# Kernel optimization log

Measured on AMD Instinct MI355X. Metric: run time of the kernel, lower is better.

The kernel has to match this reference:

```python
import jax, jax.numpy as jnp
import numpy as np

FACTOR = 1  # init factor -> top_k = int(factor * log(L))


def setup_inputs() -> dict:
    key = jax.random.key(0)
    kq, kk, kv = jax.random.split(key, 3)
    B, L, H, E = 16, 2048, 8, 64
    shape = (B, L, H, E)
    return {
        "queries": jax.random.normal(kq, shape, dtype=jnp.float32),
        "keys": jax.random.normal(kk, shape, dtype=jnp.float32),
        "values": jax.random.normal(kv, shape, dtype=jnp.float32),
    }


def reference(queries, keys, values):
    B, L, H, E = queries.shape
    # seq lens equal -> torch's pad/truncate branch is a no-op slice
    q = jnp.transpose(queries, (0, 2, 3, 1))  # [B,H,E,L]
    k = jnp.transpose(keys, (0, 2, 3, 1))
    v = jnp.transpose(values, (0, 2, 3, 1))

    # FFT-based circular cross-correlation along time
    qf = jnp.fft.rfft(q, axis=-1)
    kf = jnp.fft.rfft(k, axis=-1)
    corr = jnp.fft.irfft(qf * jnp.conj(kf), n=L, axis=-1)  # [B,H,E,L]

    top_k = int(FACTOR * np.log(L))  # static: 7 for L=2048
    mean_value = corr.mean(axis=(1, 2))  # mean over head then variates -> [B,L]
    # global (batch-averaged) top-k delays, shared across batch (training path)
    _, topk_index = jax.lax.top_k(mean_value.mean(axis=0), top_k)  # [k]
    # per-batch weights at those delays, softmax over k
    w = jax.nn.softmax(mean_value[:, topk_index], axis=-1)  # [B,k]

    # torch.roll(v, -d, -1)[..., t] == v[..., (t + d) % L]
    idx = (jnp.arange(L)[None, :] + topk_index[:, None]) % L  # [k,L]
    gathered = v[..., idx]  # [B,H,E,k,L]
    agg = jnp.einsum('bhekl,bk->bhel', gathered, w)  # weighted delay aggregation

    return jnp.transpose(agg, (0, 3, 1, 2))  # back to [B,L,H,E]
```

## Files before the change

kernel.cpp:

```cpp
#include <hip/hip_runtime.h>
#include <hip/hip_bf16.h>
#include <hip/hip_fp16.h>
#include <math.h>


#define B_ 16
#define L_ 2048
#define H_ 8
#define E_ 64
#define K_ 7
#define RS_ 2178

#define Z_OFF    0ull
#define PART_OFF 67108864ull
#define S_OFF    (PART_OFF + 33554432ull)
#define MV_OFF   (S_OFF + 262144ull)
#define TK_OFF   (MV_OFF + 131072ull)
#define W_OFF    (TK_OFF + 64ull)

__device__ __forceinline__ float2 cadd(float2 a, float2 b) { return make_float2(a.x + b.x, a.y + b.y); }
__device__ __forceinline__ float2 csub(float2 a, float2 b) { return make_float2(a.x - b.x, a.y - b.y); }
__device__ __forceinline__ float2 cmul(float2 a, float2 b) {
  return make_float2(fmaf(a.x, b.x, -a.y * b.y), fmaf(a.x, b.y, a.y * b.x));
}
__device__ __forceinline__ float2 cis(float ang) { float s, c; sincosf(ang, &s, &c); return make_float2(c, s); }

template<int S> __device__ __forceinline__ float2 rot90(float2 z) {
  return (S < 0) ? make_float2(z.y, -z.x) : make_float2(-z.y, z.x);
}
template<int S> __device__ __forceinline__ void dft4(float2& a, float2& b, float2& c, float2& d) {
  float2 t0 = cadd(a, c), t1 = csub(a, c), t2 = cadd(b, d), t3 = rot90<S>(csub(b, d));
  a = cadd(t0, t2); c = csub(t0, t2); b = cadd(t1, t3); d = csub(t1, t3);
}
template<int S> __device__ __forceinline__ void dft8(float2 v[8]) {
  const float RT = 0.70710678118654752f;
  const float SR = (S < 0) ? -RT : RT;
  float2 a0 = cadd(v[0], v[4]), a1 = cadd(v[1], v[5]), a2 = cadd(v[2], v[6]), a3 = cadd(v[3], v[7]);
  float2 b0 = csub(v[0], v[4]), b1 = csub(v[1], v[5]), b2 = csub(v[2], v[6]), b3 = csub(v[3], v[7]);
  b1 = cmul(b1, make_float2(RT, SR));
  b2 = rot90<S>(b2);
  b3 = cmul(b3, make_float2(-RT, SR));
  dft4<S>(a0, a1, a2, a3);
  dft4<S>(b0, b1, b2, b3);
  v[0] = a0; v[2] = a1; v[4] = a2; v[6] = a3;
  v[1] = b0; v[3] = b1; v[5] = b2; v[7] = b3;
}
__device__ __forceinline__ int sg(int e) { return e + (e >> 4); }

struct hc { __half2 re, im; };
__device__ __forceinline__ hc hcadd(hc a, hc b) { return { __hadd2(a.re, b.re), __hadd2(a.im, b.im) }; }
__device__ __forceinline__ hc hcsub(hc a, hc b) { return { __hsub2(a.re, b.re), __hsub2(a.im, b.im) }; }
template<int S> __device__ __forceinline__ hc hrot90(hc z) {
  hc r; if (S < 0) { r.re = z.im; r.im = __hneg2(z.re); } else { r.re = __hneg2(z.im); r.im = z.re; }
  return r;
}
__device__ __forceinline__ hc hcmul(hc v, __half2 wre, __half2 wim) {
  hc r;
  r.re = __hsub2(__hmul2(v.re, wre), __hmul2(v.im, wim));
  r.im = __hfma2(v.re, wim, __hmul2(v.im, wre));
  return r;
}
template<int S> __device__ __forceinline__ void hdft4(hc& a, hc& b, hc& c, hc& d) {
  hc t0 = hcadd(a, c), t1 = hcsub(a, c), t2 = hcadd(b, d), t3 = hrot90<S>(hcsub(b, d));
  a = hcadd(t0, t2); c = hcsub(t0, t2); b = hcadd(t1, t3); d = hcsub(t1, t3);
}
template<int S> __device__ __forceinline__ void hdft8(hc v[8]) {
  const float RT = 0.70710678118654752f;
  __half2 rt  = __float2half2_rn(RT);
  __half2 sr  = __float2half2_rn((S < 0) ? -RT : RT);
  __half2 nrt = __float2half2_rn(-RT);
  hc a0 = hcadd(v[0], v[4]), a1 = hcadd(v[1], v[5]), a2 = hcadd(v[2], v[6]), a3 = hcadd(v[3], v[7]);
  hc b0 = hcsub(v[0], v[4]), b1 = hcsub(v[1], v[5]), b2 = hcsub(v[2], v[6]), b3 = hcsub(v[3], v[7]);
  b1 = hcmul(b1, rt, sr);
  b2 = hrot90<S>(b2);
  b3 = hcmul(b3, nrt, sr);
  hdft4<S>(a0, a1, a2, a3);
  hdft4<S>(b0, b1, b2, b3);
  v[0] = a0; v[2] = a1; v[4] = a2; v[6] = a3;
  v[1] = b0; v[3] = b1; v[5] = b2; v[7] = b3;
}
__device__ __forceinline__ __half2 u2h(unsigned u) { return __builtin_bit_cast(__half2, u); }
__device__ __forceinline__ unsigned h2u(__half2 h) { return __builtin_bit_cast(unsigned, h); }

__global__ __launch_bounds__(512) void pack_kernel(
    const float* __restrict__ q, const float* __restrict__ k,
    float4* __restrict__ z) {
  int tid = threadIdx.x;
  int l = blockIdx.x;
  int tl = l & 63, b = l >> 6;
  size_t rowbase = ((size_t)b * L_ + tl * 32) * 512;
  const float4* q4 = (const float4*)(q + rowbase);
  const float4* k4 = (const float4*)(k + rowbase);
  float4* slab = z + (size_t)l * 4096;
  int w = tid >> 6;
  int lane = tid & 63;
  int r = lane >> 3, c = lane & 7;
  int srcLane = ((lane & 7) << 3) | (lane >> 3);
#pragma unroll
  for (int i = 0; i < 8; ++i) {
    int s = w * 8 + i;
    int tr = s & 3, cc = s >> 2;
    int ridx = (tr * 8 + r) * 128 + cc * 8 + c;
    float4 qv = q4[ridx];
    float4 kv = k4[ridx];
    float4 pk;
    ((__half2*)&pk)[0] = __float22half2_rn(make_float2(qv.x, qv.y));
    ((__half2*)&pk)[1] = __float22half2_rn(make_float2(kv.x, kv.y));
    ((__half2*)&pk)[2] = __float22half2_rn(make_float2(qv.z, qv.w));
    ((__half2*)&pk)[3] = __float22half2_rn(make_float2(kv.z, kv.w));
    float4 tp;
    tp.x = __shfl(pk.x, srcLane, 64);
    tp.y = __shfl(pk.y, srcLane, 64);
    tp.z = __shfl(pk.z, srcLane, 64);
    tp.w = __shfl(pk.w, srcLane, 64);
    slab[(cc * 8 + (lane >> 3)) * 32 + tr * 8 + (lane & 7)] = tp;
  }
}

__global__ __launch_bounds__(256, 4) void fft_corr_kernel(
    const float4* __restrict__ z, float2* __restrict__ part) {
  extern __shared__ uint2 dbuf[];
  int t = threadIdx.x;
  int j2 = t & 31, j3 = t & 3;
  int l = blockIdx.x;
  int cg = l & 127, b = l >> 7;
  const float4* zb = z + (size_t)b * 64 * 4096;

#pragma unroll
  for (int it = 0; it < 8; ++it) {
    int m = it * 256 + t;
    int tl = m >> 5, j = m & 31;
    float4 pk = zb[(size_t)tl * 4096 + cg * 32 + j];
    int sp = sg(tl * 32 + j);
    dbuf[sp]       = make_uint2(__float_as_uint(pk.x), __float_as_uint(pk.y));
    dbuf[RS_ + sp] = make_uint2(__float_as_uint(pk.z), __float_as_uint(pk.w));
  }

  __half2 t1re[7], t1im[7], t2re[7], t2im[7], t3re[7], t3im[7];
  {
    float2 w1 = cis(-6.283185307179586f * (float)t  / 2048.0f);
    float2 w2 = cis(-6.283185307179586f * (float)j2 / 256.0f);
    float2 w3 = cis(-6.283185307179586f * (float)j3 / 32.0f);
    float2 a1 = w1, a2 = w2, a3 = w3;
#pragma unroll
    for (int kk = 0; kk < 7; ++kk) {
      t1re[kk] = __float2half2_rn(a1.x); t1im[kk] = __float2half2_rn(a1.y);
      t2re[kk] = __float2half2_rn(a2.x); t2im[kk] = __float2half2_rn(a2.y);
      t3re[kk] = __float2half2_rn(a3.x); t3im[kk] = __float2half2_rn(a3.y);
      a1 = cmul(a1, w1); a2 = cmul(a2, w2); a3 = cmul(a3, w3);
    }
  }
  int base2 = (t >> 5) * 256 + j2;
  int base3 = (t >> 2) * 32 + j3;
  uint2* R0 = dbuf;
  uint2* R1 = dbuf + RS_;
  hc v0[8], v1[8];
  __syncthreads();

#pragma unroll
  for (int m = 0; m < 8; ++m) {
    uint2 u = R0[sg(t + 256 * m)]; v0[m].re = u2h(u.x); v0[m].im = u2h(u.y);
    u = R1[sg(t + 256 * m)];       v1[m].re = u2h(u.x); v1[m].im = u2h(u.y);
  }
  hdft8<-1>(v0); hdft8<-1>(v1);
#pragma unroll
  for (int kk = 1; kk < 8; ++kk) {
    v0[kk] = hcmul(v0[kk], t1re[kk - 1], t1im[kk - 1]);
    v1[kk] = hcmul(v1[kk], t1re[kk - 1], t1im[kk - 1]);
  }
#pragma unroll
  for (int kk = 0; kk < 8; ++kk) {
    R0[sg(t + 256 * kk)] = make_uint2(h2u(v0[kk].re), h2u(v0[kk].im));
    R1[sg(t + 256 * kk)] = make_uint2(h2u(v1[kk].re), h2u(v1[kk].im));
  }
  __syncthreads();
#pragma unroll
  for (int m = 0; m < 8; ++m) {
    uint2 u = R0[sg(base2 + 32 * m)]; v0[m].re = u2h(u.x); v0[m].im = u2h(u.y);
    u = R1[sg(base2 + 32 * m)];       v1[m].re = u2h(u.x); v1[m].im = u2h(u.y);
  }
  hdft8<-1>(v0); hdft8<-1>(v1);
#pragma unroll
  for (int kk = 1; kk < 8; ++kk) {
    v0[kk] = hcmul(v0[kk], t2re[kk - 1], t2im[kk - 1]);
    v1[kk] = hcmul(v1[kk], t2re[kk - 1], t2im[kk - 1]);
  }
#pragma unroll
  for (int kk = 0; kk < 8; ++kk) {
    R0[sg(base2 + 32 * kk)] = make_uint2(h2u(v0[kk].re), h2u(v0[kk].im));
    R1[sg(base2 + 32 * kk)] = make_uint2(h2u(v1[kk].re), h2u(v1[kk].im));
  }
  __syncthreads();
#pragma unroll
  for (int m = 0; m < 8; ++m) {
    uint2 u = R0[sg(base3 + 4 * m)]; v0[m].re = u2h(u.x); v0[m].im = u2h(u.y);
    u = R1[sg(base3 + 4 * m)];       v1[m].re = u2h(u.x); v1[m].im = u2h(u.y);
  }
  hdft8<-1>(v0); hdft8<-1>(v1);
#pragma unroll
  for (int kk = 1; kk < 8; ++kk) {
    v0[kk] = hcmul(v0[kk], t3re[kk - 1], t3im[kk - 1]);
    v1[kk] = hcmul(v1[kk], t3re[kk - 1], t3im[kk - 1]);
  }
#pragma unroll
  for (int kk = 0; kk < 8; ++kk) {
    R0[sg(base3 + 4 * kk)] = make_uint2(h2u(v0[kk].re), h2u(v0[kk].im));
    R1[sg(base3 + 4 * kk)] = make_uint2(h2u(v1[kk].re), h2u(v1[kk].im));
  }
  __syncthreads();
#pragma unroll
  for (int kk = 0; kk < 8; ++kk) {
    uint2 u = R0[sg(8 * t + kk)]; v0[kk].re = u2h(u.x); v0[kk].im = u2h(u.y);
    u = R1[sg(8 * t + kk)];       v1[kk].re = u2h(u.x); v1[kk].im = u2h(u.y);
  }
  hdft4<-1>(v0[0], v0[1], v0[2], v0[3]); hdft4<-1>(v0[4], v0[5], v0[6], v0[7]);
  hdft4<-1>(v1[0], v1[1], v1[2], v1[3]); hdft4<-1>(v1[4], v1[5], v1[6], v1[7]);
#pragma unroll
  for (int kk = 0; kk < 8; ++kk) {
    R0[sg(8 * t + kk)] = make_uint2(h2u(v0[kk].re), h2u(v0[kk].im));
    R1[sg(8 * t + kk)] = make_uint2(h2u(v1[kk].re), h2u(v1[kk].im));
  }
  __syncthreads();
  float2 acc[8];
#pragma unroll
  for (int kk = 0; kk < 8; ++kk) {
    int pos = 8 * t + kk;
    int f  = ((pos >> 8) & 7) | (((pos >> 5) & 7) << 3) | (((pos >> 2) & 7) << 6) | ((pos & 3) << 9);
    int fp = (2048 - f) & 2047;
    int pp = ((fp & 7) << 8) | (((fp >> 3) & 7) << 5) | (((fp >> 6) & 7) << 2) | ((fp >> 9) & 3);
    float sx = 0.f, sy = 0.f;
    {
      uint2 ub = R0[sg(pp)];
      __half2 bre = u2h(ub.x), bim = u2h(ub.y);
      float ar0 = __low2float(v0[kk].re),  ar1 = __high2float(v0[kk].re);
      float ai0 = __low2float(v0[kk].im),  ai1 = __high2float(v0[kk].im);
      float br0 = __low2float(bre),        br1 = __high2float(bre);
      float bi0 = __low2float(bim),        bi1 = __high2float(bim);
      sx += (br0 * ai0 + bi0 * ar0) + (br1 * ai1 + bi1 * ar1);
      sy += (ar0 * ar0 + ai0 * ai0 - br0 * br0 - bi0 * bi0)
          + (ar1 * ar1 + ai1 * ai1 - br1 * br1 - bi1 * bi1);
    }
    {
      uint2 ub = R1[sg(pp)];
      __half2 bre = u2h(ub.x), bim = u2h(ub.y);
      float ar0 = __low2float(v1[kk].re),  ar1 = __high2float(v1[kk].re);
      float ai0 = __low2float(v1[kk].im),  ai1 = __high2float(v1[kk].im);
      float br0 = __low2float(bre),        br1 = __high2float(bre);
      float bi0 = __low2float(bim),        bi1 = __high2float(bim);
      sx += (br0 * ai0 + bi0 * ar0) + (br1 * ai1 + bi1 * ar1);
      sy += (ar0 * ar0 + ai0 * ai0 - br0 * br0 - bi0 * bi0)
          + (ar1 * ar1 + ai1 * ai1 - br1 * br1 - bi1 * bi1);
    }
    acc[kk] = make_float2(0.5f * sx, 0.25f * sy);
  }
  __syncthreads();
  {
    float2* pk0 = (float2*)dbuf;
#pragma unroll
    for (int kk = 0; kk < 8; ++kk) pk0[sg(8 * t + kk)] = acc[kk];
  }
  __syncthreads();
  {
    const float2* pk0 = (const float2*)dbuf;
    float2* prow = part + (size_t)l * L_;
#pragma unroll
    for (int m = 0; m < 8; ++m) {
      int p = t + 256 * m;
      prow[p] = pk0[sg(p)];
    }
  }
}

__global__ __launch_bounds__(256) void reduce_S_kernel(
    const float2* __restrict__ part, float2* __restrict__ S) {
  int idx = blockIdx.x * 256 + threadIdx.x;
  int p = idx & 2047;
  int b = idx >> 11;
  float2 s = make_float2(0.f, 0.f);
#pragma unroll 4
  for (int i = 0; i < 128; ++i) {
    float2 vv = part[(size_t)(b * 128 + i) * L_ + p];
    s.x += vv.x; s.y += vv.y;
  }
  S[idx] = s;
}

__global__ __launch_bounds__(256) void ifft_kernel(
    const float2* __restrict__ S, float* __restrict__ mv) {
  __shared__ float2 buf[2176];
  int t = threadIdx.x, b = blockIdx.x;
  int j2 = t & 31, j3 = t & 3;
  float2 tw1[7], tw2[7], tw3[7];
  {
    float2 w1 = cis(6.283185307179586f * (float)t  / 2048.0f);
    float2 w2 = cis(6.283185307179586f * (float)j2 / 256.0f);
    float2 w3 = cis(6.283185307179586f * (float)j3 / 32.0f);
    tw1[0] = w1; tw2[0] = w2; tw3[0] = w3;
#pragma unroll
    for (int kk = 1; kk < 7; ++kk) {
      tw1[kk] = cmul(tw1[kk - 1], w1);
      tw2[kk] = cmul(tw2[kk - 1], w2);
      tw3[kk] = cmul(tw3[kk - 1], w3);
    }
  }
  int base2 = (t >> 5) * 256 + j2;
  int base3 = (t >> 2) * 32 + j3;
  float2 u[8];
  {
    const float4* rp = (const float4*)(S + (size_t)b * L_);
#pragma unroll
    for (int m = 0; m < 4; ++m) {
      float4 f = rp[4 * t + m];
      u[2 * m]     = make_float2(f.x, f.y);
      u[2 * m + 1] = make_float2(f.z, f.w);
    }
  }
  dft4<1>(u[0], u[1], u[2], u[3]);
  dft4<1>(u[4], u[5], u[6], u[7]);
#pragma unroll
  for (int kk = 0; kk < 8; ++kk) buf[sg(8 * t + kk)] = u[kk];
  __syncthreads();
  float2 v[8];
#pragma unroll
  for (int kk = 0; kk < 8; ++kk) v[kk] = buf[sg(base3 + 4 * kk)];
#pragma unroll
  for (int kk = 1; kk < 8; ++kk) v[kk] = cmul(v[kk], tw3[kk - 1]);
  dft8<1>(v);
  __syncthreads();
#pragma unroll
  for (int m = 0; m < 8; ++m) buf[sg(base3 + 4 * m)] = v[m];
  __syncthreads();
#pragma unroll
  for (int kk = 0; kk < 8; ++kk) v[kk] = buf[sg(base2 + 32 * kk)];
#pragma unroll
  for (int kk = 1; kk < 8; ++kk) v[kk] = cmul(v[kk], tw2[kk - 1]);
  dft8<1>(v);
  __syncthreads();
#pragma unroll
  for (int m = 0; m < 8; ++m) buf[sg(base2 + 32 * m)] = v[m];
  __syncthreads();
#pragma unroll
  for (int kk = 0; kk < 8; ++kk) v[kk] = buf[sg(t + 256 * kk)];
#pragma unroll
  for (int kk = 1; kk < 8; ++kk) v[kk] = cmul(v[kk], tw1[kk - 1]);
  dft8<1>(v);
  const float scale = 1.0f / (2048.0f * 512.0f);
#pragma unroll
  for (int m = 0; m < 8; ++m) mv[b * L_ + t + 256 * m] = v[m].x * scale;
}

__global__ __launch_bounds__(256) void topk_kernel(
    const float* __restrict__ mv, int* __restrict__ topk, float* __restrict__ wts) {
  __shared__ float av[2048];
  __shared__ float rv[256];
  __shared__ int   ri[256];
  __shared__ int   sidx[K_];
  int tid = threadIdx.x;
  for (int d = tid; d < 2048; d += 256) {
    float s = 0.f;
#pragma unroll
    for (int b = 0; b < B_; ++b) s += mv[b * L_ + d];
    av[d] = s;
  }
  __syncthreads();
  for (int kk = 0; kk < K_; ++kk) {
    float bv = -INFINITY; int bi = 0;
    for (int d = tid; d < 2048; d += 256) {
      float vv = av[d];
      if (vv > bv) { bv = vv; bi = d; }
    }
    rv[tid] = bv; ri[tid] = bi;
    __syncthreads();
    for (int off = 128; off > 0; off >>= 1) {
      if (tid < off) {
        float v2 = rv[tid + off]; int i2 = ri[tid + off];
        if (v2 > rv[tid] || (v2 == rv[tid] && i2 < ri[tid])) { rv[tid] = v2; ri[tid] = i2; }
      }
      __syncthreads();
    }
    if (tid == 0) { sidx[kk] = ri[0]; av[ri[0]] = -INFINITY; }
    __syncthreads();
  }
  if (tid < K_) topk[tid] = sidx[tid];
  if (tid < B_) {
    float xk[K_], m = -INFINITY;
#pragma unroll
    for (int kk = 0; kk < K_; ++kk) { xk[kk] = mv[tid * L_ + sidx[kk]]; m = fmaxf(m, xk[kk]); }
    float s = 0.f;
#pragma unroll
    for (int kk = 0; kk < K_; ++kk) { xk[kk] = expf(xk[kk] - m); s += xk[kk]; }
#pragma unroll
    for (int kk = 0; kk < K_; ++kk) wts[tid * K_ + kk] = xk[kk] / s;
  }
}

__global__ __launch_bounds__(256) void aggregate_kernel(
    const float4* __restrict__ v4, const int* __restrict__ topk,
    const float* __restrict__ wts, float4* __restrict__ out4) {
  __shared__ int   sidx[K_];
  __shared__ float sw[B_][K_];
  int tid = threadIdx.x;
  if (tid < K_) sidx[tid] = topk[tid];
  if (tid < B_ * K_) sw[tid / K_][tid % K_] = wts[tid];
  __syncthreads();
  int idx = blockIdx.x * 256 + tid;
  int c4  = idx & 127;
  int row = idx >> 7;
  int t   = row & (L_ - 1);
  int b   = row >> 11;
  float4 acc = make_float4(0.f, 0.f, 0.f, 0.f);
#pragma unroll
  for (int kk = 0; kk < K_; ++kk) {
    int s = t + sidx[kk];
    if (s >= L_) s -= L_;
    float w = sw[b][kk];
    float4 val = v4[((size_t)(b * L_ + s) << 7) + c4];
    acc.x += w * val.x; acc.y += w * val.y;
    acc.z += w * val.z; acc.w += w * val.w;
  }
  out4[idx] = acc;
}

extern "C" void kernel_launch(void* const* d_in, const int* in_sizes, int n_in,
                              void* d_out, int out_size, void* d_ws, size_t ws_size,
                              hipStream_t stream) {
  const float* q = (const float*)d_in[0];
  const float* k = (const float*)d_in[1];
  const float* v = (const float*)d_in[2];
  float* out = (float*)d_out;

  char* ws = (char*)d_ws;
  float4* z    = (float4*)(ws + Z_OFF);
  float2* part = (float2*)(ws + PART_OFF);
  float2* S    = (float2*)(ws + S_OFF);
  float*  mv   = (float*) (ws + MV_OFF);
  int*    topk = (int*)   (ws + TK_OFF);
  float*  wts  = (float*) (ws + W_OFF);

  pack_kernel<<<B_ * 64, 512, 0, stream>>>(q, k, z);
  fft_corr_kernel<<<B_ * 128, 256, 2 * RS_ * sizeof(uint2), stream>>>(z, part);
  reduce_S_kernel<<<(B_ * L_) / 256, 256, 0, stream>>>(part, S);
  ifft_kernel<<<B_, 256, 0, stream>>>(S, mv);
  topk_kernel<<<1, 256, 0, stream>>>(mv, topk, wts);
  aggregate_kernel<<<(B_ * L_ * H_ * E_ / 4) / 256, 256, 0, stream>>>(
      (const float4*)v, topk, wts, (float4*)out);
}
```

Baseline: 153.2 us.

## Pack q/k to fp16 in natural layout and remap FFT block order for locality

The pack kernel drops its shuffle-based transpose into per-tile slabs. It now writes the packed fp16 q/k data in the original [B,L,H*E] order with a simple coalesced elementwise loop. The FFT kernel reads each channel group's time series with a stride of 128 float4 per time step. Its block index is remapped so that concurrently scheduled blocks share nearby channel groups, improving cache reuse of the strided reads. This trades a cheaper pack pass for less coalesced gathers in the FFT load phase.

```diff
diff --git a/kernel.cpp b/kernel.cpp
--- a/kernel.cpp
+++ b/kernel.cpp
@@ -82,38 +82,23 @@
 __device__ __forceinline__ __half2 u2h(unsigned u) { return __builtin_bit_cast(__half2, u); }
 __device__ __forceinline__ unsigned h2u(__half2 h) { return __builtin_bit_cast(unsigned, h); }
 
-__global__ __launch_bounds__(512) void pack_kernel(
+__global__ __launch_bounds__(256) void pack_kernel(
     const float* __restrict__ q, const float* __restrict__ k,
     float4* __restrict__ z) {
-  int tid = threadIdx.x;
-  int l = blockIdx.x;
-  int tl = l & 63, b = l >> 6;
-  size_t rowbase = ((size_t)b * L_ + tl * 32) * 512;
-  const float4* q4 = (const float4*)(q + rowbase);
-  const float4* k4 = (const float4*)(k + rowbase);
-  float4* slab = z + (size_t)l * 4096;
-  int w = tid >> 6;
-  int lane = tid & 63;
-  int r = lane >> 3, c = lane & 7;
-  int srcLane = ((lane & 7) << 3) | (lane >> 3);
-#pragma unroll
-  for (int i = 0; i < 8; ++i) {
-    int s = w * 8 + i;
-    int tr = s & 3, cc = s >> 2;
-    int ridx = (tr * 8 + r) * 128 + cc * 8 + c;
-    float4 qv = q4[ridx];
-    float4 kv = k4[ridx];
+  const float4* q4 = (const float4*)q;
+  const float4* k4 = (const float4*)k;
+  int idx0 = blockIdx.x * 256 + threadIdx.x;
+#pragma unroll
+  for (int it = 0; it < 8; ++it) {
+    int idx = idx0 + it * (2048 * 256);
+    float4 qv = q4[idx];
+    float4 kv = k4[idx];
     float4 pk;
     ((__half2*)&pk)[0] = __float22half2_rn(make_float2(qv.x, qv.y));
     ((__half2*)&pk)[1] = __float22half2_rn(make_float2(kv.x, kv.y));
     ((__half2*)&pk)[2] = __float22half2_rn(make_float2(qv.z, qv.w));
     ((__half2*)&pk)[3] = __float22half2_rn(make_float2(kv.z, kv.w));
-    float4 tp;
-    tp.x = __shfl(pk.x, srcLane, 64);
-    tp.y = __shfl(pk.y, srcLane, 64);
-    tp.z = __shfl(pk.z, srcLane, 64);
-    tp.w = __shfl(pk.w, srcLane, 64);
-    slab[(cc * 8 + (lane >> 3)) * 32 + tr * 8 + (lane & 7)] = tp;
+    z[idx] = pk;
   }
 }
 
@@ -122,16 +107,17 @@
   extern __shared__ uint2 dbuf[];
   int t = threadIdx.x;
   int j2 = t & 31, j3 = t & 3;
-  int l = blockIdx.x;
+  int pphys = blockIdx.x;
+  int i = pphys >> 3, x = pphys & 7;
+  int l = ((i >> 2) << 5) | (x << 2) | (i & 3);
   int cg = l & 127, b = l >> 7;
-  const float4* zb = z + (size_t)b * 64 * 4096;
+  const float4* zb = z + (size_t)b * L_ * 128;
 
 #pragma unroll
   for (int it = 0; it < 8; ++it) {
-    int m = it * 256 + t;
-    int tl = m >> 5, j = m & 31;
-    float4 pk = zb[(size_t)tl * 4096 + cg * 32 + j];
-    int sp = sg(tl * 32 + j);
+    int tau = it * 256 + t;
+    float4 pk = zb[(size_t)tau * 128 + cg];
+    int sp = sg(tau);
     dbuf[sp]       = make_uint2(__float_as_uint(pk.x), __float_as_uint(pk.y));
     dbuf[RS_ + sp] = make_uint2(__float_as_uint(pk.z), __float_as_uint(pk.w));
   }
@@ -437,7 +423,7 @@
   int*    topk = (int*)   (ws + TK_OFF);
   float*  wts  = (float*) (ws + W_OFF);
 
-  pack_kernel<<<B_ * 64, 512, 0, stream>>>(q, k, z);
+  pack_kernel<<<2048, 256, 0, stream>>>(q, k, z);
   fft_corr_kernel<<<B_ * 128, 256, 2 * RS_ * sizeof(uint2), stream>>>(z, part);
   reduce_S_kernel<<<(B_ * L_) / 256, 256, 0, stream>>>(part, S);
   ifft_kernel<<<B_, 256, 0, stream>>>(S, mv);
```

Result: slower. 160.1 us (+4.5%).
